# Optimization experiments

Measured on AMD Instinct MI355X. Metric: run time of the kernel, lower is better.

## Reference

```python
import jax, jax.numpy as jnp
import numpy as np

B, T, C = 4, 2048, 1024
H = 16
D = C // H  # head_dim = 64


def setup_inputs() -> dict:
    key = jax.random.key(0)
    ks = jax.random.split(key, 5)
    scale_in = 1.0 / np.sqrt(C)
    x = jax.random.normal(ks[0], (B, T, C), dtype=jnp.float32)
    w_qkv = jax.random.normal(ks[1], (C, 3 * C), dtype=jnp.float32) * scale_in
    b_qkv = jnp.zeros((3 * C,), dtype=jnp.float32)
    w_proj = jax.random.normal(ks[2], (C, C), dtype=jnp.float32) * scale_in
    b_proj = jnp.zeros((C,), dtype=jnp.float32)
    return {"x": x, "w_qkv": w_qkv, "b_qkv": b_qkv, "w_proj": w_proj, "b_proj": b_proj}


def reference(x, w_qkv, b_qkv, w_proj, b_proj):
    # fused QKV projection: [B,T,3C]
    qkv = x @ w_qkv + b_qkv
    q, k, v = jnp.split(qkv, 3, axis=-1)
    # [B,T,C] -> [B,H,T,D]
    q = q.reshape(B, T, H, D).transpose(0, 2, 1, 3)
    k = k.reshape(B, T, H, D).transpose(0, 2, 1, 3)
    v = v.reshape(B, T, H, D).transpose(0, 2, 1, 3)
    scale = 1.0 / np.sqrt(D)
    scores = jnp.einsum('bhqd,bhkd->bhqk', q, k) * scale  # [B,H,T,T]
    causal = jnp.tril(jnp.ones((T, T), dtype=bool))
    scores = jnp.where(causal, scores, jnp.finfo(scores.dtype).min)
    attn = jax.nn.softmax(scores, axis=-1)
    y = jnp.einsum('bhqk,bhkd->bhqd', attn, v)  # [B,H,T,D]
    y = y.transpose(0, 2, 1, 3).reshape(B, T, C)
    return y @ w_proj + b_proj
```

## Files before the change

### kernel.cpp

```cpp
#include <hip/hip_runtime.h>

typedef unsigned short u16;
typedef unsigned int u32;
typedef unsigned long long u64;
typedef __attribute__((ext_vector_type(8))) short s16x8;
typedef __attribute__((ext_vector_type(4))) float f32x4;

#if __has_builtin(__builtin_amdgcn_exp2f)
#define EXP2(x) __builtin_amdgcn_exp2f(x)
#else
#define EXP2(x) __expf((x) * 0.69314718f)
#endif

#if __has_builtin(__builtin_amdgcn_rcpf)
#define RCP(x) __builtin_amdgcn_rcpf(x)
#else
#define RCP(x) (1.0f / (x))
#endif

#define GLL(gp, lp) __builtin_amdgcn_global_load_lds(                         \
    (const __attribute__((address_space(1))) unsigned int*)(const void*)(gp), \
    (__attribute__((address_space(3))) unsigned int*)(void*)(lp), 16, 0, 0)

__device__ __forceinline__ u16 f2bf(float f) {
    union { float f; u32 u; } v; v.f = f;
    u32 r = v.u + 0x7FFF + ((v.u >> 16) & 1);
    return (u16)(r >> 16);
}

__device__ __forceinline__ u32 pack2_trunc(float a, float b) {
    union { float f; u32 u; } x, y; x.f = a; y.f = b;
    return (x.u >> 16) | (y.u & 0xFFFF0000u);
}

__device__ __forceinline__ float bf2f(u16 b) {
    union { u32 u; float f; } v; v.u = ((u32)b) << 16;
    return v.f;
}

__device__ __forceinline__ s16x8 scale_frag(s16x8 v, float s) {
    s16x8 o;
#pragma unroll
    for (int i = 0; i < 8; i++) o[i] = (short)f2bf(bf2f((u16)v[i]) * s);
    return o;
}

__global__ __launch_bounds__(256) void cast_f32_bf16(const float* __restrict__ in,
                                                     u16* __restrict__ out) {
    size_t i = ((size_t)blockIdx.x * 256 + threadIdx.x) * 4;
    float4 f = *(const float4*)(in + i);
    u16 o[4] = { f2bf(f.x), f2bf(f.y), f2bf(f.z), f2bf(f.w) };
    *(unsigned long long*)(out + i) =
        (unsigned long long)o[0] | ((unsigned long long)o[1] << 16) |
        ((unsigned long long)o[2] << 32) | ((unsigned long long)o[3] << 48);
}

__global__ __launch_bounds__(256) void transpose_cast(const float* __restrict__ in,
                                                      u16* __restrict__ out,
                                                      int rows, int cols) {
    __shared__ float tile[32][33];
    int c0 = blockIdx.x * 32, r0 = blockIdx.y * 32;
    int tx = threadIdx.x, ty = threadIdx.y;
    for (int i = 0; i < 32; i += 8)
        tile[ty + i][tx] = in[(size_t)(r0 + ty + i) * cols + (c0 + tx)];
    __syncthreads();
    for (int i = 0; i < 32; i += 8)
        out[(size_t)(c0 + ty + i) * rows + (r0 + tx)] = f2bf(tile[tx][ty + i]);
}

template<int MODE, int NB>
__global__ __launch_bounds__(256, 4) void gemm_bt64(const u16* __restrict__ A,
                                                    const u16* __restrict__ BT,
                                                    const float* __restrict__ bias,
                                                    void* __restrict__ O1,
                                                    u16* __restrict__ vT,
                                                    int M, int N, int K) {
    __shared__ u16 SMEM[18432];
    u16* As = SMEM;
    u16* Bs = SMEM + 8192;
    int id = blockIdx.x;
    int xcd = id & 7, s = id >> 3;
    int ni = s % NB, mi8 = s / NB;
    int n0 = ni * 128, m0 = (xcd * 8 + mi8) * 128;
    int tid = threadIdx.x, lane = tid & 63, w = tid >> 6;
    int row16 = lane & 15, quad = lane >> 4;
    int wm = (w >> 1) * 64, wn = (w & 1) * 64;
    f32x4 acc[4][4] = {};

    int lr = lane >> 3;
    int cswz = (lane & 7) ^ lr;
    const u16* Ag = A + (size_t)(m0 + w * 32 + lr) * K + cswz * 8;
    const u16* Bg = BT + (size_t)(n0 + w * 32 + lr) * K + cswz * 8;
    u16* Asl = As + (w * 32) * 64;
    u16* Bsl = Bs + (w * 32) * 64;

    for (int k0 = 0; k0 < K; k0 += 64) {
        __syncthreads();
#pragma unroll
        for (int j = 0; j < 4; j++) {
            GLL(Ag + k0 + (size_t)j * 8 * K, Asl + j * 8 * 64);
            GLL(Bg + k0 + (size_t)j * 8 * K, Bsl + j * 8 * 64);
        }
        __syncthreads();
#pragma unroll
        for (int kk = 0; kk < 2; kk++) {
            s16x8 af[4], bf[4];
#pragma unroll
            for (int mi = 0; mi < 4; mi++)
                af[mi] = *(const s16x8*)&As[(wm + mi * 16 + row16) * 64 +
                                            (((kk * 4 + quad) ^ (row16 & 7)) * 8)];
#pragma unroll
            for (int ni2 = 0; ni2 < 4; ni2++)
                bf[ni2] = *(const s16x8*)&Bs[(wn + ni2 * 16 + row16) * 64 +
                                             (((kk * 4 + quad) ^ (row16 & 7)) * 8)];
#pragma unroll
            for (int mi = 0; mi < 4; mi++)
#pragma unroll
                for (int ni2 = 0; ni2 < 4; ni2++)
                    acc[mi][ni2] = __builtin_amdgcn_mfma_f32_16x16x32_bf16(
                        af[mi], bf[ni2], acc[mi][ni2], 0, 0, 0);
        }
    }

    if (MODE == 0) {
        float* O = (float*)O1;
#pragma unroll
        for (int ni2 = 0; ni2 < 4; ni2++) {
            int col = n0 + wn + ni2 * 16 + row16;
            float bv = bias[col];
#pragma unroll
            for (int mi = 0; mi < 4; mi++)
#pragma unroll
                for (int r = 0; r < 4; r++)
                    O[(size_t)(m0 + wm + mi * 16 + quad * 4 + r) * N + col] =
                        acc[mi][ni2][r] + bv;
        }
    } else if (n0 < 2048) {
        u16* qk = (u16*)O1;
#pragma unroll
        for (int ni2 = 0; ni2 < 4; ni2++) {
            int col = n0 + wn + ni2 * 16 + row16;
            float bv = bias[col];
#pragma unroll
            for (int mi = 0; mi < 4; mi++)
#pragma unroll
                for (int r = 0; r < 4; r++)
                    qk[(size_t)(m0 + wm + mi * 16 + quad * 4 + r) * 2048 + col] =
                        f2bf(acc[mi][ni2][r] + bv);
        }
    } else {
        __syncthreads();
        u16* scr = SMEM + w * 64 * 72;
#pragma unroll
        for (int ni2 = 0; ni2 < 4; ni2++) {
            float bv = bias[n0 + wn + ni2 * 16 + row16];
#pragma unroll
            for (int mi = 0; mi < 4; mi++)
#pragma unroll
                for (int r = 0; r < 4; r++)
                    scr[(ni2 * 16 + row16) * 72 + (mi * 16 + quad * 4 + r)] =
                        f2bf(acc[mi][ni2][r] + bv);
        }
        __syncthreads();
        int r8 = lane >> 3, c8 = lane & 7;
        int vbase = (m0 >> 11) * 1024 + (n0 - 2048) + wn;
        int tb = (m0 & 2047) + wm;
#pragma unroll
        for (int it = 0; it < 8; it++) {
            s16x8 vv = *(const s16x8*)&scr[(it * 8 + r8) * 72 + c8 * 8];
            *(s16x8*)&vT[(size_t)(vbase + it * 8 + r8) * 2048 + tb + c8 * 8] = vv;
        }
    }
}

__global__ __launch_bounds__(256, 2) void attn_kernel(const u16* __restrict__ qk,
                                                      const u16* __restrict__ vT,
                                                      u16* __restrict__ y) {
    __shared__ u16 Kb[2][4096];
    __shared__ u16 Vb[2][4096];
    __shared__ u16 Ps[4][2048];

    int tid = threadIdx.x, lane = tid & 63, w = tid >> 6;
    int row16 = lane & 15, quad = lane >> 4;
    int id = blockIdx.x;
    int xcd = id & 7, slot = id >> 3;
    int pairi = slot >> 3;
    int bh = ((slot & 7) << 3) | xcd;
    int b = bh >> 4, h = bh & 15;
    const u16* qkb = qk + (size_t)b * 2048 * 2048;
    const u16* vtb = vT + ((size_t)(b * 1024) + h * 64) * 2048;

    int lr = lane >> 3, cswz = (lane & 7) ^ lr;
    const u16* Kg = qkb + (size_t)(w * 16 + lr) * 2048 + 1024 + h * 64 + cswz * 8;
    const u16* Vg = vtb + (size_t)(w * 16 + lr) * 2048 + cswz * 8;
    u16* Psw = Ps[w];
    int sw = row16 & 7;

    s16x8 ones;
#pragma unroll
    for (int i = 0; i < 8; i++) ones[i] = (short)0x3F80;
    const float qs = 0.125f * 1.44269504f;

    for (int half = 0; half < 2; half++) {
        int qt = half ? pairi : (15 - pairi);
        int q0 = qt * 128;
        int niter = 2 * qt + 2;
        int qw = q0 + w * 32;

        s16x8 qf[2][2];
#pragma unroll
        for (int mi = 0; mi < 2; mi++) {
            const u16* qp = qkb + (size_t)(qw + mi * 16 + row16) * 2048 + h * 64 + quad * 8;
            qf[mi][0] = scale_frag(*(const s16x8*)qp, qs);
            qf[mi][1] = scale_frag(*(const s16x8*)(qp + 32), qs);
        }

        f32x4 acc_o[2][4] = {};
        f32x4 acc_l[2] = {};

        __syncthreads();
#pragma unroll
        for (int j = 0; j < 2; j++) {
            GLL(Kg + (size_t)j * 8 * 2048, Kb[0] + w * 16 * 64 + j * 8 * 64);
            GLL(Vg + (size_t)j * 8 * 2048, Vb[0] + w * 16 * 64 + j * 8 * 64);
        }

        for (int kb = 0; kb < niter; kb++) {
            int cur = kb & 1;
            __syncthreads();
            if (kb + 1 < niter) {
                int k1 = (kb + 1) * 64;
#pragma unroll
                for (int j = 0; j < 2; j++) {
                    GLL(Kg + (size_t)(k1 + j * 8) * 2048, Kb[cur ^ 1] + w * 16 * 64 + j * 8 * 64);
                    GLL(Vg + k1 + (size_t)j * 8 * 2048, Vb[cur ^ 1] + w * 16 * 64 + j * 8 * 64);
                }
            }
            int k0 = kb * 64;
            if (k0 > qw + 31) continue;
            const u16* Kc = Kb[cur];
            const u16* Vc = Vb[cur];

            f32x4 sc[2][4];
#pragma unroll
            for (int nk = 0; nk < 4; nk++) {
                s16x8 kf0 = *(const s16x8*)&Kc[(nk * 16 + row16) * 64 + ((quad ^ sw) * 8)];
                s16x8 kf1 = *(const s16x8*)&Kc[(nk * 16 + row16) * 64 + (((4 + quad) ^ sw) * 8)];
#pragma unroll
                for (int mi = 0; mi < 2; mi++) {
                    f32x4 z = {};
                    z = __builtin_amdgcn_mfma_f32_16x16x32_bf16(kf0, qf[mi][0], z, 0, 0, 0);
                    z = __builtin_amdgcn_mfma_f32_16x16x32_bf16(kf1, qf[mi][1], z, 0, 0, 0);
                    sc[mi][nk] = z;
                }
            }
            if (k0 + 63 > qw) {
#pragma unroll
                for (int mi = 0; mi < 2; mi++) {
                    int qg = qw + mi * 16 + row16;
#pragma unroll
                    for (int nk = 0; nk < 4; nk++) {
                        int kbase = k0 + nk * 16 + quad * 4;
#pragma unroll
                        for (int r = 0; r < 4; r++)
                            if (kbase + r > qg) sc[mi][nk][r] = -__builtin_inff();
                    }
                }
            }
#pragma unroll
            for (int mi = 0; mi < 2; mi++)
#pragma unroll
                for (int nk = 0; nk < 4; nk++) {
                    float p0 = EXP2(sc[mi][nk][0]);
                    float p1 = EXP2(sc[mi][nk][1]);
                    float p2 = EXP2(sc[mi][nk][2]);
                    float p3 = EXP2(sc[mi][nk][3]);
                    u32 w0 = pack2_trunc(p0, p1);
                    u32 w1 = pack2_trunc(p2, p3);
                    int u = nk * 2 + (quad >> 1);
                    int eo = ((u ^ sw) * 8) + (quad & 1) * 4;
                    *(u64*)&Psw[mi * 1024 + row16 * 64 + eo] = (u64)w0 | ((u64)w1 << 32);
                }
#pragma unroll
            for (int kk = 0; kk < 2; kk++) {
                int co = ((kk * 4 + quad) ^ sw) * 8;
                s16x8 pf0 = *(const s16x8*)&Psw[row16 * 64 + co];
                s16x8 pf1 = *(const s16x8*)&Psw[1024 + row16 * 64 + co];
#pragma unroll
                for (int nd = 0; nd < 4; nd++) {
                    s16x8 vf = *(const s16x8*)&Vc[(nd * 16 + row16) * 64 + co];
                    acc_o[0][nd] = __builtin_amdgcn_mfma_f32_16x16x32_bf16(pf0, vf, acc_o[0][nd], 0, 0, 0);
                    acc_o[1][nd] = __builtin_amdgcn_mfma_f32_16x16x32_bf16(pf1, vf, acc_o[1][nd], 0, 0, 0);
                }
                acc_l[0] = __builtin_amdgcn_mfma_f32_16x16x32_bf16(pf0, ones, acc_l[0], 0, 0, 0);
                acc_l[1] = __builtin_amdgcn_mfma_f32_16x16x32_bf16(pf1, ones, acc_l[1], 0, 0, 0);
            }
        }

#pragma unroll
        for (int mi = 0; mi < 2; mi++) {
            int t0 = qw + mi * 16 + quad * 4;
#pragma unroll
            for (int r = 0; r < 4; r++) {
                float inv = RCP(acc_l[mi][r]);
#pragma unroll
                for (int nd = 0; nd < 4; nd++)
                    y[((size_t)b * 2048 + t0 + r) * 1024 + h * 64 + nd * 16 + row16] =
                        f2bf(acc_o[mi][nd][r] * inv);
            }
        }
    }
}

extern "C" void kernel_launch(void* const* d_in, const int* in_sizes, int n_in,
                              void* d_out, int out_size, void* d_ws, size_t ws_size,
                              hipStream_t stream) {
    const float* x      = (const float*)d_in[0];
    const float* w_qkv  = (const float*)d_in[1];
    const float* b_qkv  = (const float*)d_in[2];
    const float* w_proj = (const float*)d_in[3];
    const float* b_proj = (const float*)d_in[4];
    float* out = (float*)d_out;

    u16* ws     = (u16*)d_ws;
    u16* x_bf   = ws;
    u16* wqkvT  = x_bf  + (size_t)8192 * 1024;
    u16* wprojT = wqkvT + (size_t)3072 * 1024;
    u16* qkbuf  = wprojT + (size_t)1024 * 1024;
    u16* vT     = qkbuf + (size_t)8192 * 2048;
    u16* ybf    = vT    + (size_t)4096 * 2048;

    cast_f32_bf16<<<dim3(8192), dim3(256), 0, stream>>>(x, x_bf);
    transpose_cast<<<dim3(96, 32), dim3(32, 8), 0, stream>>>(w_qkv, wqkvT, 1024, 3072);
    transpose_cast<<<dim3(32, 32), dim3(32, 8), 0, stream>>>(w_proj, wprojT, 1024, 1024);
    gemm_bt64<1, 24><<<dim3(1536), 256, 0, stream>>>(x_bf, wqkvT, b_qkv, (void*)qkbuf, vT, 8192, 3072, 1024);
    attn_kernel<<<dim3(512), 256, 0, stream>>>(qkbuf, vT, ybf);
    gemm_bt64<0, 8><<<dim3(512), 256, 0, stream>>>(ybf, wprojT, b_proj, (void*)out, nullptr, 8192, 1024, 1024);
}
```

Before: 230.7 us.

## Retile attention to 64-row query tiles, fuse prep kernels, simplify GEMM grid

The attention kernel now uses 128-thread blocks (two waves) over 64-row query tiles, with 1024 blocks. Query tiles are still paired heavy with light to balance the causal work. Each wave loads 32 K/V rows per stage, and the P scratch shrinks to match. The cast and two transpose-cast kernels are merged into one launch to cut launch overhead. The GEMMs drop the XCD-aware block remapping in favour of a plain 2D grid, which may give up some L2 locality across chiplets.

```diff
diff --git a/kernel.cpp b/kernel.cpp
--- a/kernel.cpp
+++ b/kernel.cpp
@@ -45,30 +45,42 @@
     return o;
 }
 
-__global__ __launch_bounds__(256) void cast_f32_bf16(const float* __restrict__ in,
-                                                     u16* __restrict__ out) {
-    size_t i = ((size_t)blockIdx.x * 256 + threadIdx.x) * 4;
-    float4 f = *(const float4*)(in + i);
-    u16 o[4] = { f2bf(f.x), f2bf(f.y), f2bf(f.z), f2bf(f.w) };
-    *(unsigned long long*)(out + i) =
-        (unsigned long long)o[0] | ((unsigned long long)o[1] << 16) |
-        ((unsigned long long)o[2] << 32) | ((unsigned long long)o[3] << 48);
-}
-
-__global__ __launch_bounds__(256) void transpose_cast(const float* __restrict__ in,
-                                                      u16* __restrict__ out,
-                                                      int rows, int cols) {
+__global__ __launch_bounds__(256) void prep(const float* __restrict__ x,
+                                            const float* __restrict__ w_qkv,
+                                            const float* __restrict__ w_proj,
+                                            u16* __restrict__ x_bf,
+                                            u16* __restrict__ wqkvT,
+                                            u16* __restrict__ wprojT) {
+    int id = blockIdx.x, tid = threadIdx.x;
+    if (id < 8192) {
+        size_t i = ((size_t)id * 256 + tid) * 4;
+        float4 f = *(const float4*)(x + i);
+        u16 o[4] = { f2bf(f.x), f2bf(f.y), f2bf(f.z), f2bf(f.w) };
+        *(u64*)(x_bf + i) = (u64)o[0] | ((u64)o[1] << 16) | ((u64)o[2] << 32) |
+                            ((u64)o[3] << 48);
+        return;
+    }
     __shared__ float tile[32][33];
-    int c0 = blockIdx.x * 32, r0 = blockIdx.y * 32;
-    int tx = threadIdx.x, ty = threadIdx.y;
+    const float* in; u16* out; int rows, cols, bx, by;
+    if (id < 11264) {
+        int blk = id - 8192; bx = blk % 96; by = blk / 96;
+        in = w_qkv; out = wqkvT; rows = 1024; cols = 3072;
+    } else {
+        int blk = id - 11264; bx = blk & 31; by = blk >> 5;
+        in = w_proj; out = wprojT; rows = 1024; cols = 1024;
+    }
+    int c0 = bx * 32, r0 = by * 32;
+    int tx = tid & 31, ty = tid >> 5;
+#pragma unroll
     for (int i = 0; i < 32; i += 8)
         tile[ty + i][tx] = in[(size_t)(r0 + ty + i) * cols + (c0 + tx)];
     __syncthreads();
+#pragma unroll
     for (int i = 0; i < 32; i += 8)
         out[(size_t)(c0 + ty + i) * rows + (r0 + tx)] = f2bf(tile[tx][ty + i]);
 }
 
-template<int MODE, int NB>
+template<int MODE>
 __global__ __launch_bounds__(256, 4) void gemm_bt64(const u16* __restrict__ A,
                                                     const u16* __restrict__ BT,
                                                     const float* __restrict__ bias,
@@ -78,10 +90,7 @@
     __shared__ u16 SMEM[18432];
     u16* As = SMEM;
     u16* Bs = SMEM + 8192;
-    int id = blockIdx.x;
-    int xcd = id & 7, s = id >> 3;
-    int ni = s % NB, mi8 = s / NB;
-    int n0 = ni * 128, m0 = (xcd * 8 + mi8) * 128;
+    int n0 = blockIdx.x * 128, m0 = blockIdx.y * 128;
     int tid = threadIdx.x, lane = tid & 63, w = tid >> 6;
     int row16 = lane & 15, quad = lane >> 4;
     int wm = (w >> 1) * 64, wn = (w & 1) * 64;
@@ -110,56 +119,56 @@
                 af[mi] = *(const s16x8*)&As[(wm + mi * 16 + row16) * 64 +
                                             (((kk * 4 + quad) ^ (row16 & 7)) * 8)];
 #pragma unroll
-            for (int ni2 = 0; ni2 < 4; ni2++)
-                bf[ni2] = *(const s16x8*)&Bs[(wn + ni2 * 16 + row16) * 64 +
-                                             (((kk * 4 + quad) ^ (row16 & 7)) * 8)];
-#pragma unroll
-            for (int mi = 0; mi < 4; mi++)
-#pragma unroll
-                for (int ni2 = 0; ni2 < 4; ni2++)
-                    acc[mi][ni2] = __builtin_amdgcn_mfma_f32_16x16x32_bf16(
-                        af[mi], bf[ni2], acc[mi][ni2], 0, 0, 0);
+            for (int ni = 0; ni < 4; ni++)
+                bf[ni] = *(const s16x8*)&Bs[(wn + ni * 16 + row16) * 64 +
+                                            (((kk * 4 + quad) ^ (row16 & 7)) * 8)];
+#pragma unroll
+            for (int mi = 0; mi < 4; mi++)
+#pragma unroll
+                for (int ni = 0; ni < 4; ni++)
+                    acc[mi][ni] = __builtin_amdgcn_mfma_f32_16x16x32_bf16(
+                        af[mi], bf[ni], acc[mi][ni], 0, 0, 0);
         }
     }
 
     if (MODE == 0) {
         float* O = (float*)O1;
 #pragma unroll
-        for (int ni2 = 0; ni2 < 4; ni2++) {
-            int col = n0 + wn + ni2 * 16 + row16;
+        for (int ni = 0; ni < 4; ni++) {
+            int col = n0 + wn + ni * 16 + row16;
             float bv = bias[col];
 #pragma unroll
             for (int mi = 0; mi < 4; mi++)
 #pragma unroll
                 for (int r = 0; r < 4; r++)
                     O[(size_t)(m0 + wm + mi * 16 + quad * 4 + r) * N + col] =
-                        acc[mi][ni2][r] + bv;
+                        acc[mi][ni][r] + bv;
         }
     } else if (n0 < 2048) {
         u16* qk = (u16*)O1;
 #pragma unroll
-        for (int ni2 = 0; ni2 < 4; ni2++) {
-            int col = n0 + wn + ni2 * 16 + row16;
+        for (int ni = 0; ni < 4; ni++) {
+            int col = n0 + wn + ni * 16 + row16;
             float bv = bias[col];
 #pragma unroll
             for (int mi = 0; mi < 4; mi++)
 #pragma unroll
                 for (int r = 0; r < 4; r++)
                     qk[(size_t)(m0 + wm + mi * 16 + quad * 4 + r) * 2048 + col] =
-                        f2bf(acc[mi][ni2][r] + bv);
+                        f2bf(acc[mi][ni][r] + bv);
         }
     } else {
         __syncthreads();
         u16* scr = SMEM + w * 64 * 72;
 #pragma unroll
-        for (int ni2 = 0; ni2 < 4; ni2++) {
-            float bv = bias[n0 + wn + ni2 * 16 + row16];
+        for (int ni = 0; ni < 4; ni++) {
+            float bv = bias[n0 + wn + ni * 16 + row16];
 #pragma unroll
             for (int mi = 0; mi < 4; mi++)
 #pragma unroll
                 for (int r = 0; r < 4; r++)
-                    scr[(ni2 * 16 + row16) * 72 + (mi * 16 + quad * 4 + r)] =
-                        f2bf(acc[mi][ni2][r] + bv);
+                    scr[(ni * 16 + row16) * 72 + (mi * 16 + quad * 4 + r)] =
+                        f2bf(acc[mi][ni][r] + bv);
         }
         __syncthreads();
         int r8 = lane >> 3, c8 = lane & 7;
@@ -173,12 +182,12 @@
     }
 }
 
-__global__ __launch_bounds__(256, 2) void attn_kernel(const u16* __restrict__ qk,
+__global__ __launch_bounds__(128, 2) void attn_kernel(const u16* __restrict__ qk,
                                                       const u16* __restrict__ vT,
                                                       u16* __restrict__ y) {
     __shared__ u16 Kb[2][4096];
     __shared__ u16 Vb[2][4096];
-    __shared__ u16 Ps[4][2048];
+    __shared__ u16 Ps[2][2048];
 
     int tid = threadIdx.x, lane = tid & 63, w = tid >> 6;
     int row16 = lane & 15, quad = lane >> 4;
@@ -191,8 +200,8 @@
     const u16* vtb = vT + ((size_t)(b * 1024) + h * 64) * 2048;
 
     int lr = lane >> 3, cswz = (lane & 7) ^ lr;
-    const u16* Kg = qkb + (size_t)(w * 16 + lr) * 2048 + 1024 + h * 64 + cswz * 8;
-    const u16* Vg = vtb + (size_t)(w * 16 + lr) * 2048 + cswz * 8;
+    const u16* Kg = qkb + (size_t)(w * 32 + lr) * 2048 + 1024 + h * 64 + cswz * 8;
+    const u16* Vg = vtb + (size_t)(w * 32 + lr) * 2048 + cswz * 8;
     u16* Psw = Ps[w];
     int sw = row16 & 7;
 
@@ -202,9 +211,9 @@
     const float qs = 0.125f * 1.44269504f;
 
     for (int half = 0; half < 2; half++) {
-        int qt = half ? pairi : (15 - pairi);
-        int q0 = qt * 128;
-        int niter = 2 * qt + 2;
+        int qt = half ? pairi : (31 - pairi);
+        int q0 = qt * 64;
+        int niter = qt + 1;
         int qw = q0 + w * 32;
 
         s16x8 qf[2][2];
@@ -220,9 +229,9 @@
 
         __syncthreads();
 #pragma unroll
-        for (int j = 0; j < 2; j++) {
-            GLL(Kg + (size_t)j * 8 * 2048, Kb[0] + w * 16 * 64 + j * 8 * 64);
-            GLL(Vg + (size_t)j * 8 * 2048, Vb[0] + w * 16 * 64 + j * 8 * 64);
+        for (int j = 0; j < 4; j++) {
+            GLL(Kg + (size_t)j * 8 * 2048, Kb[0] + w * 32 * 64 + j * 8 * 64);
+            GLL(Vg + (size_t)j * 8 * 2048, Vb[0] + w * 32 * 64 + j * 8 * 64);
         }
 
         for (int kb = 0; kb < niter; kb++) {
@@ -231,9 +240,9 @@
             if (kb + 1 < niter) {
                 int k1 = (kb + 1) * 64;
 #pragma unroll
-                for (int j = 0; j < 2; j++) {
-                    GLL(Kg + (size_t)(k1 + j * 8) * 2048, Kb[cur ^ 1] + w * 16 * 64 + j * 8 * 64);
-                    GLL(Vg + k1 + (size_t)j * 8 * 2048, Vb[cur ^ 1] + w * 16 * 64 + j * 8 * 64);
+                for (int j = 0; j < 4; j++) {
+                    GLL(Kg + (size_t)(k1 + j * 8) * 2048, Kb[cur ^ 1] + w * 32 * 64 + j * 8 * 64);
+                    GLL(Vg + k1 + (size_t)j * 8 * 2048, Vb[cur ^ 1] + w * 32 * 64 + j * 8 * 64);
                 }
             }
             int k0 = kb * 64;
@@ -330,10 +339,8 @@
     u16* vT     = qkbuf + (size_t)8192 * 2048;
     u16* ybf    = vT    + (size_t)4096 * 2048;
 
-    cast_f32_bf16<<<dim3(8192), dim3(256), 0, stream>>>(x, x_bf);
-    transpose_cast<<<dim3(96, 32), dim3(32, 8), 0, stream>>>(w_qkv, wqkvT, 1024, 3072);
-    transpose_cast<<<dim3(32, 32), dim3(32, 8), 0, stream>>>(w_proj, wprojT, 1024, 1024);
-    gemm_bt64<1, 24><<<dim3(1536), 256, 0, stream>>>(x_bf, wqkvT, b_qkv, (void*)qkbuf, vT, 8192, 3072, 1024);
-    attn_kernel<<<dim3(512), 256, 0, stream>>>(qkbuf, vT, ybf);
-    gemm_bt64<0, 8><<<dim3(512), 256, 0, stream>>>(ybf, wprojT, b_proj, (void*)out, nullptr, 8192, 1024, 1024);
-}
+    prep<<<dim3(12288), 256, 0, stream>>>(x, w_qkv, w_proj, x_bf, wqkvT, wprojT);
+    gemm_bt64<1><<<dim3(24, 64), 256, 0, stream>>>(x_bf, wqkvT, b_qkv, (void*)qkbuf, vT, 8192, 3072, 1024);
+    attn_kernel<<<dim3(1024), 128, 0, stream>>>(qkbuf, vT, ybf);
+    gemm_bt64<0><<<dim3(8, 64), 256, 0, stream>>>(ybf, wprojT, b_proj, (void*)out, nullptr, 8192, 1024, 1024);
+}
```

After: 238.7 us. 1.03x slower.
